# Kernel optimization log

Hardware: AMD Instinct MI355X
Metric: run time of the kernel (lower is better)

## Reference

```python
import jax, jax.numpy as jnp
import numpy as np

B, Q, K, D, H = 4, 2048, 2048, 512, 8
HD = D // H
_INF = -1e30


def setup_inputs() -> dict:
    key = jax.random.key(0)
    ks = jax.random.split(key, 8)
    scale = 1.0 / HD ** 0.5
    return {
        "query": jax.random.normal(ks[0], (B, Q, D), jnp.float32),
        "key": jax.random.normal(ks[1], (B, K, D), jnp.float32),
        "value": jax.random.normal(ks[2], (B, K, D), jnp.float32),
        "Wq": jax.random.normal(ks[3], (D, D), jnp.float32) * scale,  # [out,in]
        "Wk": jax.random.normal(ks[4], (D, D), jnp.float32) * scale,
        "Wv": jax.random.normal(ks[5], (D, D), jnp.float32) * scale,
        "Wo": jax.random.normal(ks[6], (D, D), jnp.float32) * scale,
        "attn_mask": jax.random.randint(ks[7], (B, K), 0, 2, jnp.int32),
    }


def reference(query, key, value, Wq, Wk, Wv, Wo, attn_mask):
    bsz, qlen, _ = query.shape
    klen = key.shape[1]
    head_q = (query @ Wq.T).reshape(bsz, qlen, H, HD)
    head_k = (key @ Wk.T).reshape(bsz, klen, H, HD)
    head_v = (value @ Wv.T).reshape(bsz, klen, H, HD)
    scale = 1.0 / HD ** 0.5
    # [b, i, j, n] score tensor, as in the torch einsum 'bind,bjnd->bijn'
    attn_score = jnp.einsum('bind,bjnd->bijn', head_q, head_k) * scale
    mask = (attn_mask == 0)[:, None, :, None]  # dim-2 mask branch
    attn_score = jnp.where(mask, _INF, attn_score)
    attn_prob = jax.nn.softmax(attn_score, axis=2)  # softmax over key axis j
    attn_vec = jnp.einsum('bijn,bjnd->bind', attn_prob, head_v)
    attn_vec = attn_vec.reshape(bsz, qlen, H * HD)
    return attn_vec @ Wo.T
```

## Files before the change

### kernel.cpp

```cpp
#include <hip/hip_runtime.h>

constexpr int Bc   = 4;
constexpr int Qlen = 2048;
constexpr int Klen = 2048;
constexpr int Dm   = 512;
constexpr int Hh   = 8;
constexpr int HDim = 64;
constexpr float C1 = 0.125f * 1.4426950408889634f;

typedef __attribute__((ext_vector_type(8))) short short8;
typedef __attribute__((ext_vector_type(8))) _Float16 half8;
typedef __attribute__((ext_vector_type(2))) __fp16 fp16x2;
typedef __attribute__((ext_vector_type(4))) float f32x4;

__device__ __forceinline__ f32x4 MFMA16(short8 a, short8 b, f32x4 c) {
  return __builtin_amdgcn_mfma_f32_16x16x32_f16(
      __builtin_bit_cast(half8, a), __builtin_bit_cast(half8, b), c, 0, 0, 0);
}

__device__ __forceinline__ void gload_lds16(const void* g, void* l) {
  __builtin_amdgcn_global_load_lds(
      (const __attribute__((address_space(1))) void*)g,
      (__attribute__((address_space(3))) void*)l, 16, 0, 0);
}

__device__ __forceinline__ unsigned short f2h(float f) {
  _Float16 h = (_Float16)f;
  return __builtin_bit_cast(unsigned short, h);
}

__device__ __forceinline__ unsigned pk2h(float a, float b) {
  fp16x2 h = __builtin_amdgcn_cvt_pkrtz(a, b);
  return __builtin_bit_cast(unsigned, h);
}

__global__ __launch_bounds__(256) void scan_mask(
    const int* __restrict__ msk, int* __restrict__ idx, int* __restrict__ cnt) {
  const int b = blockIdx.x;
  const int tid = threadIdx.x;
  __shared__ int wtot[4];
  const int* mrow = msk + b * Klen;
  int m8[8];
  int c = 0;
#pragma unroll
  for (int i = 0; i < 8; ++i) {
    m8[i] = mrow[tid * 8 + i];
    c += (m8[i] != 0);
  }
  int pre = c;
#pragma unroll
  for (int off = 1; off < 64; off <<= 1) {
    int t = __shfl_up(pre, off);
    if ((tid & 63) >= off) pre += t;
  }
  const int w = tid >> 6;
  if ((tid & 63) == 63) wtot[w] = pre;
  __syncthreads();
  int base = 0;
  for (int i = 0; i < w; ++i) base += wtot[i];
  int p = base + pre - c;
#pragma unroll
  for (int i = 0; i < 8; ++i)
    if (m8[i] != 0) idx[b * Klen + (p++)] = tid * 8 + i;
  if (tid == 255) cnt[b] = base + pre;
}

__global__ __launch_bounds__(256) void cvt4(
    const float* __restrict__ s0, const float* __restrict__ s1,
    const float* __restrict__ s2, const float* __restrict__ s3,
    unsigned short* __restrict__ o0, unsigned short* __restrict__ o1,
    unsigned short* __restrict__ o2, unsigned short* __restrict__ o3,
    const int* __restrict__ msk, float* __restrict__ biasf) {
  const int seg = blockIdx.y;
  int i = (blockIdx.x * 256 + threadIdx.x) * 4;
  if (seg < 4) {
    const float* s = (seg == 0) ? s0 : (seg == 1) ? s1 : (seg == 2) ? s2 : s3;
    unsigned short* o = (seg == 0) ? o0 : (seg == 1) ? o1 : (seg == 2) ? o2 : o3;
    float4 x = *(const float4*)(s + i);
    unsigned t[2] = {pk2h(x.x, x.y), pk2h(x.z, x.w)};
    *(uint2*)(o + i) = *(const uint2*)t;
  } else if (i + 3 < Bc * Klen) {
    int4 m = *(const int4*)(msk + i);
    float4 bo;
    bo.x = (m.x == 0) ? -60000.0f : 0.0f;
    bo.y = (m.y == 0) ? -60000.0f : 0.0f;
    bo.z = (m.z == 0) ? -60000.0f : 0.0f;
    bo.w = (m.w == 0) ? -60000.0f : 0.0f;
    *(float4*)(biasf + i) = bo;
  }
}

__global__ __launch_bounds__(256) void cvt_in(
    const float* __restrict__ q, const float* __restrict__ k,
    const float* __restrict__ v,
    unsigned short* __restrict__ qh, unsigned short* __restrict__ kh,
    unsigned short* __restrict__ vh,
    const int* __restrict__ idx, const int* __restrict__ cnt) {
  const int seg = blockIdx.y;
  int g = blockIdx.x * 256 + threadIdx.x;
  int i = g * 4;
  if (seg == 0) {
    float4 x = *(const float4*)(q + i);
    unsigned t[2] = {pk2h(x.x, x.y), pk2h(x.z, x.w)};
    *(uint2*)(qh + i) = *(const uint2*)t;
    return;
  }
  const float* s = (seg == 1) ? k : v;
  unsigned short* o = (seg == 1) ? kh : vh;
  int row = i >> 9, col = i & 511;
  int b = row >> 11, jc = row & 2047;
  int cb = cnt[b];
  if (jc < cb) {
    int j = idx[b * Klen + jc];
    float4 x = *(const float4*)(s + ((size_t)(b * Klen + j)) * 512 + col);
    unsigned t[2] = {pk2h(x.x, x.y), pk2h(x.z, x.w)};
    *(uint2*)(o + (size_t)row * 512 + col) = *(const uint2*)t;
  } else if (jc < ((cb + 127) & ~127)) {
    uint2 z = {0u, 0u};
    *(uint2*)(o + (size_t)row * 512 + col) = z;
  }
}

template <bool F16A>
__global__ __launch_bounds__(256) void gemm_qkv(
    const float* __restrict__ q_in,
    const float* __restrict__ k_in,
    const float* __restrict__ v_in,
    const unsigned short* __restrict__ qh,
    const unsigned short* __restrict__ kh,
    const unsigned short* __restrict__ vh,
    const unsigned short* __restrict__ Wqh,
    const unsigned short* __restrict__ Wkh,
    const unsigned short* __restrict__ Wvh,
    unsigned short* __restrict__ Qp,
    unsigned short* __restrict__ Kp,
    unsigned short* __restrict__ Vp,
    const int* __restrict__ cnt) {
  __shared__ unsigned short As[2][128 * 32];
  __shared__ unsigned short Bs[2][128 * 32];
  const int tid = threadIdx.x;
  const int w = tid >> 6, l = tid & 63;
  const int quad = l >> 4, l15 = l & 15;
  const int m0 = blockIdx.x * 128;
  const int n0 = blockIdx.y * 128;
  const int seg = n0 >> 9;
  const int f0  = n0 & 511;
  if constexpr (F16A) {
    if (seg != 0) {
      int local = m0 & 2047;
      if (local >= ((cnt[m0 >> 11] + 63) & ~63)) return;
    }
  }
  const float* Af = (seg == 0) ? q_in : (seg == 1) ? k_in : v_in;
  const unsigned short* Ah = (seg == 0) ? qh : (seg == 1) ? kh : vh;
  const unsigned short* W = (seg == 0) ? Wqh : (seg == 1) ? Wkh : Wvh;
  unsigned short* dst = (seg == 0) ? Qp : (seg == 1) ? Kp : Vp;

  f32x4 acc[4][4] = {};
  const int lrow = l >> 2;
  const int lcol = (l & 3) * 8;
  const int wm = (w >> 1) * 64, wn = (w & 1) * 64;

  auto stage = [&](int bs, int kk) {
#pragma unroll
    for (int i = 0; i < 2; ++i) {
      int row = w * 32 + i * 16 + lrow;
      if constexpr (F16A) {
        gload_lds16(Ah + (size_t)(m0 + row) * 512 + kk + lcol, &As[bs][row * 32 + lcol]);
      } else {
        const float* ap = Af + (size_t)(m0 + row) * 512 + kk + lcol;
        float4 x0 = *(const float4*)(ap);
        float4 x1 = *(const float4*)(ap + 4);
        unsigned t[4] = {pk2h(x0.x, x0.y), pk2h(x0.z, x0.w),
                         pk2h(x1.x, x1.y), pk2h(x1.z, x1.w)};
        *(uint4*)&As[bs][row * 32 + lcol] = *(const uint4*)t;
      }
      gload_lds16(W + (size_t)(f0 + row) * 512 + kk + lcol, &Bs[bs][row * 32 + lcol]);
    }
  };

  stage(0, 0);
  for (int kk = 0; kk < 512; kk += 32) {
    const int cur = (kk >> 5) & 1;
    __syncthreads();
    if (kk + 32 < 512) stage(cur ^ 1, kk + 32);
    short8 af[4], bf[4];
#pragma unroll
    for (int t = 0; t < 4; ++t)
      af[t] = *(const short8*)&As[cur][(wm + t * 16 + l15) * 32 + quad * 8];
#pragma unroll
    for (int t = 0; t < 4; ++t)
      bf[t] = *(const short8*)&Bs[cur][(wn + t * 16 + l15) * 32 + quad * 8];
#pragma unroll
    for (int mt = 0; mt < 4; ++mt)
#pragma unroll
      for (int nt = 0; nt < 4; ++nt)
        acc[mt][nt] = MFMA16(af[mt], bf[nt], acc[mt][nt]);
  }
  const float oscale = (seg == 0) ? C1 : 1.0f;
#pragma unroll
  for (int mt = 0; mt < 4; ++mt)
#pragma unroll
    for (int nt = 0; nt < 4; ++nt)
#pragma unroll
      for (int r = 0; r < 4; ++r) {
        int m  = m0 + wm + mt * 16 + quad * 4 + r;
        int nn = f0 + wn + nt * 16 + l15;
        int b = m >> 11, qq = m & 2047;
        int h = nn >> 6, hd = nn & 63;
        dst[(((size_t)(b * Hh + h)) * Qlen + qq) * HDim + hd] =
            f2h(acc[mt][nt][r] * oscale);
      }
}

__global__ __launch_bounds__(256) void transpose_v(
    const unsigned short* __restrict__ Vp, unsigned short* __restrict__ Vt,
    const int* __restrict__ cnt) {
  __shared__ unsigned short t[64 * 72];
  const int bh = blockIdx.y, jt = blockIdx.x;
  if (cnt) {
    if (jt * 64 >= ((cnt[bh >> 3] + 63) & ~63)) return;
  }
  const int tid = threadIdx.x;
#pragma unroll
  for (int i = 0; i < 2; ++i) {
    int g = i * 256 + tid;
    int j = g >> 3, c8 = g & 7;
    *(uint4*)&t[j * 72 + c8 * 8] =
        *(const uint4*)(Vp + ((size_t)bh * Klen + jt * 64 + j) * 64 + c8 * 8);
  }
  __syncthreads();
#pragma unroll
  for (int i = 0; i < 2; ++i) {
    int g = i * 256 + tid;
    int d = g >> 3, j8 = g & 7;
    unsigned short tmp[8];
#pragma unroll
    for (int kx = 0; kx < 8; ++kx) tmp[kx] = t[(j8 * 8 + kx) * 72 + d];
    *(uint4*)(Vt + ((size_t)bh * HDim + d) * Klen + jt * 64 + j8 * 8) = *(const uint4*)tmp;
  }
}

__global__ __launch_bounds__(256) void gemm_out(
    const unsigned short* __restrict__ Oa,
    const unsigned short* __restrict__ Woh,
    float* __restrict__ out) {
  __shared__ unsigned short As[2][128 * 32];
  __shared__ unsigned short Bs[2][128 * 32];
  const int tid = threadIdx.x;
  const int w = tid >> 6, l = tid & 63;
  const int quad = l >> 4, l15 = l & 15;
  const int m0 = blockIdx.x * 128;
  const int n0 = blockIdx.y * 128;

  f32x4 acc[4][4] = {};
  const int lrow = l >> 2;
  const int lcol = (l & 3) * 8;
  const int wm = (w >> 1) * 64, wn = (w & 1) * 64;

  auto stage = [&](int bs, int kk) {
#pragma unroll
    for (int i = 0; i < 2; ++i) {
      int row = w * 32 + i * 16 + lrow;
      gload_lds16(Oa + (size_t)(m0 + row) * 512 + kk + lcol, &As[bs][row * 32 + lcol]);
      gload_lds16(Woh + (size_t)(n0 + row) * 512 + kk + lcol, &Bs[bs][row * 32 + lcol]);
    }
  };

  stage(0, 0);
  for (int kk = 0; kk < 512; kk += 32) {
    const int cur = (kk >> 5) & 1;
    __syncthreads();
    if (kk + 32 < 512) stage(cur ^ 1, kk + 32);
    short8 af[4], bf[4];
#pragma unroll
    for (int t = 0; t < 4; ++t)
      af[t] = *(const short8*)&As[cur][(wm + t * 16 + l15) * 32 + quad * 8];
#pragma unroll
    for (int t = 0; t < 4; ++t)
      bf[t] = *(const short8*)&Bs[cur][(wn + t * 16 + l15) * 32 + quad * 8];
#pragma unroll
    for (int mt = 0; mt < 4; ++mt)
#pragma unroll
      for (int nt = 0; nt < 4; ++nt)
        acc[mt][nt] = MFMA16(af[mt], bf[nt], acc[mt][nt]);
  }
#pragma unroll
  for (int mt = 0; mt < 4; ++mt)
#pragma unroll
    for (int nt = 0; nt < 4; ++nt)
#pragma unroll
      for (int r = 0; r < 4; ++r) {
        int m  = m0 + wm + mt * 16 + quad * 4 + r;
        int nn = n0 + wn + nt * 16 + l15;
        out[(size_t)m * 512 + nn] = acc[mt][nt][r];
      }
}

template <bool KSPLIT, bool COMPACT>
__global__ __launch_bounds__(512, 4) void attn(
    const unsigned short* __restrict__ Qp,
    const unsigned short* __restrict__ Kp,
    const unsigned short* __restrict__ Vt,
    const float* __restrict__ biasf,
    const int* __restrict__ cntArr,
    unsigned short* __restrict__ Oa,
    unsigned short* __restrict__ Op,
    float* __restrict__ Sp) {
  __shared__ unsigned short Ks[2][64 * 64];
  __shared__ unsigned short Vs[2][64 * 64];
  __shared__ unsigned short Ps[8][16 * 72];

  const int tid = threadIdx.x;
  const int w = tid >> 6, l = tid & 63;
  const int quad = l >> 4, l15 = l & 15;
  const int bid = blockIdx.x;
  const int bh = bid & 31;
  const int b = bh >> 3, h = bh & 7;

  int cnt, KT;
  if constexpr (COMPACT) {
    cnt = cntArr[b];
    KT = (cnt + 63) >> 6;
  } else {
    cnt = Klen;
    KT = Klen / 64;
  }

  const int qt = bid >> 5;
  const int kt0 = 0, ktN = KT;
  const int x = l15 & 7;
  const int qrow = qt * 128 + w * 16 + l15;

  short8 aq[2];
#pragma unroll
  for (int k2 = 0; k2 < 2; ++k2)
    aq[k2] = *(const short8*)(Qp + ((size_t)bh * Qlen + qrow) * HDim + (k2 * 4 + quad) * 8);

  short8 ones;
#pragma unroll
  for (int j = 0; j < 8; ++j) ones[j] = (short)0x3C00;

  f32x4 o[4] = {};
  f32x4 o5 = {};
  float m_run = -1.0e6f;
  const float* brow = biasf + b * Klen;

  auto stage = [&](int bs, int kt) {
    int g = tid;
    int row = g >> 3, c8 = g & 7;
    int sb = (c8 ^ (row & 7)) * 8;
    gload_lds16(Kp + ((size_t)bh * Klen + kt * 64 + row) * HDim + sb, &Ks[bs][g * 8]);
    gload_lds16(Vt + ((size_t)bh * HDim + row) * Klen + kt * 64 + sb, &Vs[bs][g * 8]);
  };

  stage(0, kt0);
  for (int kt = kt0; kt < ktN; ++kt) {
    const int cur = (kt - kt0) & 1;
    __syncthreads();
    if (kt + 1 < ktN) stage(cur ^ 1, kt + 1);

    float4 bb[4];
    if constexpr (!COMPACT) {
#pragma unroll
      for (int ct = 0; ct < 4; ++ct)
        bb[ct] = *(const float4*)(brow + kt * 64 + ct * 16 + quad * 4);
    }

    f32x4 sv[4];
    __builtin_amdgcn_s_setprio(1);
#pragma unroll
    for (int ct = 0; ct < 4; ++ct) {
      const short8 bk0 = *(const short8*)&Ks[cur][(ct * 16 + l15) * 64 + (quad ^ x) * 8];
      const short8 bk1 = *(const short8*)&Ks[cur][(ct * 16 + l15) * 64 + ((4 + quad) ^ x) * 8];
      f32x4 a = {};
      a = MFMA16(bk0, aq[0], a);
      a = MFMA16(bk1, aq[1], a);
      sv[ct] = a;
    }
    __builtin_amdgcn_s_setprio(0);

    if constexpr (!COMPACT) {
#pragma unroll
      for (int ct = 0; ct < 4; ++ct)
#pragma unroll
        for (int r = 0; r < 4; ++r)
          sv[ct][r] += bb[ct][r];
    } else {
      if (kt == KT - 1) {
#pragma unroll
        for (int ct = 0; ct < 4; ++ct)
#pragma unroll
          for (int r = 0; r < 4; ++r)
            if (kt * 64 + ct * 16 + quad * 4 + r >= cnt) sv[ct][r] = -60000.0f;
      }
    }

    float mx0 = fmaxf(fmaxf(sv[0][0], sv[0][1]), fmaxf(sv[0][2], sv[0][3]));
    float mx1 = fmaxf(fmaxf(sv[1][0], sv[1][1]), fmaxf(sv[1][2], sv[1][3]));
    float mx2 = fmaxf(fmaxf(sv[2][0], sv[2][1]), fmaxf(sv[2][2], sv[2][3]));
    float mx3 = fmaxf(fmaxf(sv[3][0], sv[3][1]), fmaxf(sv[3][2], sv[3][3]));
    float mx = fmaxf(fmaxf(mx0, mx1), fmaxf(mx2, mx3));
    mx = fmaxf(mx, __shfl_xor(mx, 16));
    mx = fmaxf(mx, __shfl_xor(mx, 32));
    if (__any(mx > m_run + 8.0f)) {
      float mnew  = fmaxf(m_run, mx);
      float alpha = exp2f(m_run - mnew);
      m_run = mnew;
#pragma unroll
      for (int ctd = 0; ctd < 4; ++ctd) o[ctd] *= alpha;
      o5 *= alpha;
    }

#pragma unroll
    for (int ct = 0; ct < 4; ++ct) {
      float p0 = exp2f(sv[ct][0] - m_run);
      float p1 = exp2f(sv[ct][1] - m_run);
      float p2 = exp2f(sv[ct][2] - m_run);
      float p3 = exp2f(sv[ct][3] - m_run);
      unsigned pk[2] = {pk2h(p0, p1), pk2h(p2, p3)};
      *(uint2*)&Ps[w][l15 * 72 + ct * 16 + quad * 4] = *(const uint2*)pk;
    }
    const short8 ap0 = *(const short8*)&Ps[w][l15 * 72 + quad * 8];
    const short8 ap1 = *(const short8*)&Ps[w][l15 * 72 + 32 + quad * 8];

    __builtin_amdgcn_s_setprio(1);
    o5 = MFMA16(ones, ap0, o5);
    o5 = MFMA16(ones, ap1, o5);
#pragma unroll
    for (int ctd = 0; ctd < 4; ++ctd) {
      const short8 bv0 = *(const short8*)&Vs[cur][(ctd * 16 + l15) * 64 + (quad ^ x) * 8];
      const short8 bv1 = *(const short8*)&Vs[cur][(ctd * 16 + l15) * 64 + ((4 + quad) ^ x) * 8];
      o[ctd] = MFMA16(bv0, ap0, o[ctd]);
      o[ctd] = MFMA16(bv1, ap1, o[ctd]);
    }
    __builtin_amdgcn_s_setprio(0);
  }

  float lt = o5[0];
  float rl = (lt > 0.0f) ? 1.0f / lt : 0.0f;
  const size_t obase = ((size_t)(b * Qlen) + qrow) * Dm + h * 64;
#pragma unroll
  for (int ctd = 0; ctd < 4; ++ctd) {
    unsigned pk[2] = {pk2h(o[ctd][0] * rl, o[ctd][1] * rl),
                      pk2h(o[ctd][2] * rl, o[ctd][3] * rl)};
    *(uint2*)(Oa + obase + ctd * 16 + quad * 4) = *(const uint2*)pk;
  }
}

extern "C" void kernel_launch(void* const* d_in, const int* in_sizes, int n_in,
                              void* d_out, int out_size, void* d_ws, size_t ws_size,
                              hipStream_t stream) {
  const float* q  = (const float*)d_in[0];
  const float* k  = (const float*)d_in[1];
  const float* v  = (const float*)d_in[2];
  const float* Wq = (const float*)d_in[3];
  const float* Wk = (const float*)d_in[4];
  const float* Wv = (const float*)d_in[5];
  const float* Wo = (const float*)d_in[6];
  const int*  msk = (const int*)d_in[7];
  float* out = (float*)d_out;

  char* ws = (char*)d_ws;
  const size_t SEG  = (size_t)Bc * Hh * Qlen * HDim * sizeof(unsigned short);
  const size_t WSEG = (size_t)Dm * Dm * sizeof(unsigned short);
  unsigned short* Qp  = (unsigned short*)(ws);
  unsigned short* Kp  = (unsigned short*)(ws + SEG);
  unsigned short* Vp  = (unsigned short*)(ws + 2 * SEG);
  unsigned short* Vt  = (unsigned short*)(ws + 3 * SEG);
  unsigned short* Oa  = Vp;
  unsigned short* Wqh = (unsigned short*)(ws + 4 * SEG);
  unsigned short* Wkh = (unsigned short*)(ws + 4 * SEG + WSEG);
  unsigned short* Wvh = (unsigned short*)(ws + 4 * SEG + 2 * WSEG);
  unsigned short* Woh = (unsigned short*)(ws + 4 * SEG + 3 * WSEG);
  int*   idxArr = (int*)(ws + 4 * SEG + 4 * WSEG);
  int*   cntArr = idxArr + Bc * Klen;
  float* Bfs    = (float*)idxArr;
  unsigned short* qh  = (unsigned short*)(ws + 4 * SEG + 4 * WSEG + 65536);
  unsigned short* kh  = qh + SEG / 2;
  unsigned short* vh  = kh + SEG / 2;
  const size_t NEED = 4 * SEG + 4 * WSEG + 65536 + 3 * SEG;
  const bool big = ws_size >= NEED;

  auto attn_one    = attn<false, true>;
  auto attn_single = attn<false, false>;

  const int wn = Dm * Dm;
  if (big) {
    hipLaunchKernelGGL(scan_mask, dim3(Bc), dim3(256), 0, stream, msk, idxArr, cntArr);
    hipLaunchKernelGGL(cvt4, dim3(wn / 1024, 4), dim3(256), 0, stream,
                       Wq, Wk, Wv, Wo, Wqh, Wkh, Wvh, Woh, msk, Bfs);
    hipLaunchKernelGGL(cvt_in, dim3(4096, 3), dim3(256), 0, stream,
                       q, k, v, qh, kh, vh, idxArr, cntArr);
    hipLaunchKernelGGL(gemm_qkv<true>, dim3(64, 12), dim3(256), 0, stream,
                       q, k, v, qh, kh, vh, Wqh, Wkh, Wvh, Qp, Kp, Vp, cntArr);
    hipLaunchKernelGGL(transpose_v, dim3(32, 32), dim3(256), 0, stream, Vp, Vt, cntArr);
    hipLaunchKernelGGL(attn_one, dim3(512), dim3(512), 0, stream,
                       Qp, Kp, Vt, Bfs, cntArr, Oa,
                       (unsigned short*)nullptr, (float*)nullptr);
  } else {
    hipLaunchKernelGGL(cvt4, dim3(wn / 1024, 5), dim3(256), 0, stream,
                       Wq, Wk, Wv, Wo, Wqh, Wkh, Wvh, Woh, msk, Bfs);
    hipLaunchKernelGGL(gemm_qkv<false>, dim3(64, 12), dim3(256), 0, stream,
                       q, k, v, qh, kh, vh, Wqh, Wkh, Wvh, Qp, Kp, Vp, cntArr);
    hipLaunchKernelGGL(transpose_v, dim3(32, 32), dim3(256), 0, stream, Vp, Vt,
                       (const int*)nullptr);
    hipLaunchKernelGGL(attn_single, dim3(512), dim3(512), 0, stream,
                       Qp, Kp, Vt, Bfs, (const int*)nullptr, Oa,
                       (unsigned short*)nullptr, (float*)nullptr);
  }
  hipLaunchKernelGGL(gemm_out, dim3(64, 4), dim3(256), 0, stream, Oa, Woh, out);
}
```

Before: 183.1 us.

## Fuse input fp16 conversion and mask gather into QKV projection GEMM

Drops the separate cvt_in kernel that converted q/k/v to fp16 and compacted unmasked key/value rows into a scratch buffer. The QKV GEMM now reads fp32 inputs directly, follows the compaction index per row to gather K/V rows, and zero-fills padding rows in LDS. This removes one launch and a full write/read round trip of the fp16 copies. In exchange, A tiles go through register conversion instead of async global-to-LDS loads, and K/V reads become gathered rows.

```diff
diff --git a/kernel.cpp b/kernel.cpp
--- a/kernel.cpp
+++ b/kernel.cpp
@@ -121,20 +121,17 @@
   }
 }
 
-template <bool F16A>
-__global__ __launch_bounds__(256) void gemm_qkv(
+__global__ __launch_bounds__(256) void gemm_qkv_fused(
     const float* __restrict__ q_in,
     const float* __restrict__ k_in,
     const float* __restrict__ v_in,
-    const unsigned short* __restrict__ qh,
-    const unsigned short* __restrict__ kh,
-    const unsigned short* __restrict__ vh,
     const unsigned short* __restrict__ Wqh,
     const unsigned short* __restrict__ Wkh,
     const unsigned short* __restrict__ Wvh,
     unsigned short* __restrict__ Qp,
     unsigned short* __restrict__ Kp,
     unsigned short* __restrict__ Vp,
+    const int* __restrict__ idx,
     const int* __restrict__ cnt) {
   __shared__ unsigned short As[2][128 * 32];
   __shared__ unsigned short Bs[2][128 * 32];
@@ -145,14 +142,11 @@
   const int n0 = blockIdx.y * 128;
   const int seg = n0 >> 9;
   const int f0  = n0 & 511;
-  if constexpr (F16A) {
-    if (seg != 0) {
-      int local = m0 & 2047;
-      if (local >= ((cnt[m0 >> 11] + 63) & ~63)) return;
-    }
+  if (seg != 0) {
+    int local = m0 & 2047;
+    if (local >= ((cnt[m0 >> 11] + 63) & ~63)) return;
   }
   const float* Af = (seg == 0) ? q_in : (seg == 1) ? k_in : v_in;
-  const unsigned short* Ah = (seg == 0) ? qh : (seg == 1) ? kh : vh;
   const unsigned short* W = (seg == 0) ? Wqh : (seg == 1) ? Wkh : Wvh;
   unsigned short* dst = (seg == 0) ? Qp : (seg == 1) ? Kp : Vp;
 
@@ -161,20 +155,112 @@
   const int lcol = (l & 3) * 8;
   const int wm = (w >> 1) * 64, wn = (w & 1) * 64;
 
+  const float* aptr[2];
+#pragma unroll
+  for (int i = 0; i < 2; ++i) {
+    int row = w * 32 + i * 16 + lrow;
+    int m = m0 + row;
+    if (seg == 0) {
+      aptr[i] = Af + (size_t)m * 512 + lcol;
+    } else {
+      int b = m >> 11, jc = m & 2047;
+      aptr[i] = (jc < cnt[b])
+                    ? Af + ((size_t)(b * Klen + idx[b * Klen + jc])) * 512 + lcol
+                    : nullptr;
+    }
+  }
+
   auto stage = [&](int bs, int kk) {
 #pragma unroll
     for (int i = 0; i < 2; ++i) {
       int row = w * 32 + i * 16 + lrow;
-      if constexpr (F16A) {
-        gload_lds16(Ah + (size_t)(m0 + row) * 512 + kk + lcol, &As[bs][row * 32 + lcol]);
-      } else {
-        const float* ap = Af + (size_t)(m0 + row) * 512 + kk + lcol;
+      if (aptr[i]) {
+        const float* ap = aptr[i] + kk;
         float4 x0 = *(const float4*)(ap);
         float4 x1 = *(const float4*)(ap + 4);
         unsigned t[4] = {pk2h(x0.x, x0.y), pk2h(x0.z, x0.w),
                          pk2h(x1.x, x1.y), pk2h(x1.z, x1.w)};
         *(uint4*)&As[bs][row * 32 + lcol] = *(const uint4*)t;
+      } else {
+        uint4 z = {0u, 0u, 0u, 0u};
+        *(uint4*)&As[bs][row * 32 + lcol] = z;
       }
+      gload_lds16(W + (size_t)(f0 + row) * 512 + kk + lcol, &Bs[bs][row * 32 + lcol]);
+    }
+  };
+
+  stage(0, 0);
+  for (int kk = 0; kk < 512; kk += 32) {
+    const int cur = (kk >> 5) & 1;
+    __syncthreads();
+    if (kk + 32 < 512) stage(cur ^ 1, kk + 32);
+    short8 af[4], bf[4];
+#pragma unroll
+    for (int t = 0; t < 4; ++t)
+      af[t] = *(const short8*)&As[cur][(wm + t * 16 + l15) * 32 + quad * 8];
+#pragma unroll
+    for (int t = 0; t < 4; ++t)
+      bf[t] = *(const short8*)&Bs[cur][(wn + t * 16 + l15) * 32 + quad * 8];
+#pragma unroll
+    for (int mt = 0; mt < 4; ++mt)
+#pragma unroll
+      for (int nt = 0; nt < 4; ++nt)
+        acc[mt][nt] = MFMA16(af[mt], bf[nt], acc[mt][nt]);
+  }
+  const float oscale = (seg == 0) ? C1 : 1.0f;
+#pragma unroll
+  for (int mt = 0; mt < 4; ++mt)
+#pragma unroll
+    for (int nt = 0; nt < 4; ++nt)
+#pragma unroll
+      for (int r = 0; r < 4; ++r) {
+        int m  = m0 + wm + mt * 16 + quad * 4 + r;
+        int nn = f0 + wn + nt * 16 + l15;
+        int b = m >> 11, qq = m & 2047;
+        int h = nn >> 6, hd = nn & 63;
+        dst[(((size_t)(b * Hh + h)) * Qlen + qq) * HDim + hd] =
+            f2h(acc[mt][nt][r] * oscale);
+      }
+}
+
+__global__ __launch_bounds__(256) void gemm_qkv_plain(
+    const float* __restrict__ q_in,
+    const float* __restrict__ k_in,
+    const float* __restrict__ v_in,
+    const unsigned short* __restrict__ Wqh,
+    const unsigned short* __restrict__ Wkh,
+    const unsigned short* __restrict__ Wvh,
+    unsigned short* __restrict__ Qp,
+    unsigned short* __restrict__ Kp,
+    unsigned short* __restrict__ Vp) {
+  __shared__ unsigned short As[2][128 * 32];
+  __shared__ unsigned short Bs[2][128 * 32];
+  const int tid = threadIdx.x;
+  const int w = tid >> 6, l = tid & 63;
+  const int quad = l >> 4, l15 = l & 15;
+  const int m0 = blockIdx.x * 128;
+  const int n0 = blockIdx.y * 128;
+  const int seg = n0 >> 9;
+  const int f0  = n0 & 511;
+  const float* Af = (seg == 0) ? q_in : (seg == 1) ? k_in : v_in;
+  const unsigned short* W = (seg == 0) ? Wqh : (seg == 1) ? Wkh : Wvh;
+  unsigned short* dst = (seg == 0) ? Qp : (seg == 1) ? Kp : Vp;
+
+  f32x4 acc[4][4] = {};
+  const int lrow = l >> 2;
+  const int lcol = (l & 3) * 8;
+  const int wm = (w >> 1) * 64, wn = (w & 1) * 64;
+
+  auto stage = [&](int bs, int kk) {
+#pragma unroll
+    for (int i = 0; i < 2; ++i) {
+      int row = w * 32 + i * 16 + lrow;
+      const float* ap = Af + (size_t)(m0 + row) * 512 + kk + lcol;
+      float4 x0 = *(const float4*)(ap);
+      float4 x1 = *(const float4*)(ap + 4);
+      unsigned t[4] = {pk2h(x0.x, x0.y), pk2h(x0.z, x0.w),
+                       pk2h(x1.x, x1.y), pk2h(x1.z, x1.w)};
+      *(uint4*)&As[bs][row * 32 + lcol] = *(const uint4*)t;
       gload_lds16(W + (size_t)(f0 + row) * 512 + kk + lcol, &Bs[bs][row * 32 + lcol]);
     }
   };
@@ -476,10 +562,7 @@
   int*   idxArr = (int*)(ws + 4 * SEG + 4 * WSEG);
   int*   cntArr = idxArr + Bc * Klen;
   float* Bfs    = (float*)idxArr;
-  unsigned short* qh  = (unsigned short*)(ws + 4 * SEG + 4 * WSEG + 65536);
-  unsigned short* kh  = qh + SEG / 2;
-  unsigned short* vh  = kh + SEG / 2;
-  const size_t NEED = 4 * SEG + 4 * WSEG + 65536 + 3 * SEG;
+  const size_t NEED = 4 * SEG + 4 * WSEG + 65536;
   const bool big = ws_size >= NEED;
 
   auto attn_one    = attn<false, true>;
@@ -490,10 +573,8 @@
     hipLaunchKernelGGL(scan_mask, dim3(Bc), dim3(256), 0, stream, msk, idxArr, cntArr);
     hipLaunchKernelGGL(cvt4, dim3(wn / 1024, 4), dim3(256), 0, stream,
                        Wq, Wk, Wv, Wo, Wqh, Wkh, Wvh, Woh, msk, Bfs);
-    hipLaunchKernelGGL(cvt_in, dim3(4096, 3), dim3(256), 0, stream,
-                       q, k, v, qh, kh, vh, idxArr, cntArr);
-    hipLaunchKernelGGL(gemm_qkv<true>, dim3(64, 12), dim3(256), 0, stream,
-                       q, k, v, qh, kh, vh, Wqh, Wkh, Wvh, Qp, Kp, Vp, cntArr);
+    hipLaunchKernelGGL(gemm_qkv_fused, dim3(64, 12), dim3(256), 0, stream,
+                       q, k, v, Wqh, Wkh, Wvh, Qp, Kp, Vp, idxArr, cntArr);
     hipLaunchKernelGGL(transpose_v, dim3(32, 32), dim3(256), 0, stream, Vp, Vt, cntArr);
     hipLaunchKernelGGL(attn_one, dim3(512), dim3(512), 0, stream,
                        Qp, Kp, Vt, Bfs, cntArr, Oa,
@@ -501,8 +582,8 @@
   } else {
     hipLaunchKernelGGL(cvt4, dim3(wn / 1024, 5), dim3(256), 0, stream,
                        Wq, Wk, Wv, Wo, Wqh, Wkh, Wvh, Woh, msk, Bfs);
-    hipLaunchKernelGGL(gemm_qkv<false>, dim3(64, 12), dim3(256), 0, stream,
-                       q, k, v, qh, kh, vh, Wqh, Wkh, Wvh, Qp, Kp, Vp, cntArr);
+    hipLaunchKernelGGL(gemm_qkv_plain, dim3(64, 12), dim3(256), 0, stream,
+                       q, k, v, Wqh, Wkh, Wvh, Qp, Kp, Vp);
     hipLaunchKernelGGL(transpose_v, dim3(32, 32), dim3(256), 0, stream, Vp, Vt,
                        (const int*)nullptr);
     hipLaunchKernelGGL(attn_single, dim3(512), dim3(512), 0, stream,
```

Result: slower. 190.7 us (+4.2%).
